# Optimization experiments

Hardware: AMD Instinct MI355X
Metric: run time of the kernel (lower is better)

Reference implementation:

```python
import jax, jax.numpy as jnp
import numpy as np

N_NODES = 50000
N_EDGES = 800000
LEAKY_SLOPE = 0.01
DROPOUT_P = 0.5


def _graph_conv(src, dst, x, W, b):
    """DGL GraphConv with norm='both': D_out^{-1/2} A D_in^{-1/2} X W + b."""
    n = x.shape[0]
    ones = jnp.ones((src.shape[0],), dtype=x.dtype)
    deg_out = jax.ops.segment_sum(ones, src, num_segments=n)  # out-degree of src nodes
    deg_in = jax.ops.segment_sum(ones, dst, num_segments=n)   # in-degree of dst nodes
    norm_src = jax.lax.rsqrt(jnp.maximum(deg_out, 1.0))
    norm_dst = jax.lax.rsqrt(jnp.maximum(deg_in, 1.0))
    h = (x * norm_src[:, None]) @ W          # apply weight before aggregation
    agg = jax.ops.segment_sum(h[src], dst, num_segments=n)  # SpMM aggregate
    return agg * norm_dst[:, None] + b


def _dropout(x, key, p=DROPOUT_P):
    keep = jax.random.bernoulli(key, 1.0 - p, x.shape)
    return jnp.where(keep, x / (1.0 - p), jnp.zeros((), x.dtype))


def setup_inputs() -> dict:
    key = jax.random.key(0)
    ks = jax.random.split(key, 8)
    features = jax.random.normal(ks[0], (N_NODES, 128), dtype=jnp.float32)
    src = jax.random.randint(ks[1], (N_EDGES,), 0, N_NODES, dtype=jnp.int64)
    dst = jax.random.randint(ks[2], (N_EDGES,), 0, N_NODES, dtype=jnp.int64)
    s1 = 1.0 / np.sqrt(128.0)
    s3 = 1.0 / np.sqrt(128.0)
    W1 = jax.random.normal(ks[3], (128, 128), dtype=jnp.float32) * s1
    W2 = jax.random.normal(ks[4], (128, 128), dtype=jnp.float32) * s1
    W3 = jax.random.normal(ks[5], (128, 64), dtype=jnp.float32) * s3
    b1 = jnp.zeros((128,), dtype=jnp.float32)
    b2 = jnp.zeros((128,), dtype=jnp.float32)
    b3 = jnp.zeros((64,), dtype=jnp.float32)
    return {"features": features, "src": src, "dst": dst,
            "W1": W1, "b1": b1, "W2": W2, "b2": b2, "W3": W3, "b3": b3}


def reference(features, src, dst, W1, b1, W2, b2, W3, b3):
    dk = jax.random.split(jax.random.key(42), 3)
    h = jax.nn.leaky_relu(_graph_conv(src, dst, features, W1, b1), LEAKY_SLOPE)
    h = _dropout(h, dk[0])
    h = jax.nn.leaky_relu(_graph_conv(src, dst, h, W2, b2), LEAKY_SLOPE)
    h = _dropout(h, dk[1])
    h = jax.nn.leaky_relu(_graph_conv(src, dst, h, W3, b3), LEAKY_SLOPE)
    h = _dropout(h, dk[2])
    return h
```

## Files before the change

kernel.cpp:

```cpp
#include <hip/hip_runtime.h>
#include <hip/hip_fp16.h>
#include <stdint.h>

using half8 = __attribute__((ext_vector_type(8))) _Float16;
using f32x4 = __attribute__((ext_vector_type(4))) float;

#define SLOT_CAP 64
#define LDW 136
#define NBINS 50176
#define LWORDS 12544
#define NCHUNK 128

#define TFR(r) { x0 += x1; x1 = (x1 << r) | (x1 >> (32 - r)); x1 ^= x0; }

__host__ __device__ inline void threefry2x32(uint32_t k0, uint32_t k1,
                                             uint32_t c0, uint32_t c1,
                                             uint32_t& o0, uint32_t& o1) {
  uint32_t ks2 = k0 ^ k1 ^ 0x1BD11BDAu;
  uint32_t x0 = c0 + k0, x1 = c1 + k1;
  TFR(13) TFR(15) TFR(26) TFR(6)  x0 += k1;  x1 += ks2 + 1u;
  TFR(17) TFR(29) TFR(16) TFR(24) x0 += ks2; x1 += k0 + 2u;
  TFR(13) TFR(15) TFR(26) TFR(6)  x0 += k0;  x1 += k1 + 3u;
  TFR(17) TFR(29) TFR(16) TFR(24) x0 += k1;  x1 += ks2 + 4u;
  TFR(13) TFR(15) TFR(26) TFR(6)  x0 += ks2; x1 += k0 + 5u;
  o0 = x0; o1 = x1;
}

__device__ inline float tf_uniform(uint32_t k0, uint32_t k1, uint32_t i) {
  uint32_t o0, o1;
  threefry2x32(k0, k1, 0u, i, o0, o1);
  uint32_t bits = o0 ^ o1;
  return __uint_as_float((bits >> 9) | 0x3F800000u) - 1.0f;
}

__device__ inline uint16_t f2h(float f) {
  union { _Float16 h; uint16_t u; } c; c.h = (_Float16)f; return c.u;
}
__device__ inline uint32_t pack2h(float a, float b) {
  return (uint32_t)f2h(a) | ((uint32_t)f2h(b) << 16);
}
__device__ inline __half2 u2h2(uint32_t u) {
  union { uint32_t u; __half2 h; } c; c.u = u; return c.h;
}

__device__ inline void hacc(__half2* a, uint4 r) {
  a[0] = __hadd2(a[0], u2h2(r.x));
  a[1] = __hadd2(a[1], u2h2(r.y));
  a[2] = __hadd2(a[2], u2h2(r.z));
  a[3] = __hadd2(a[3], u2h2(r.w));
}

#define GDECL \
  uint4 A0, A1, A2, A3, A4, A5, A6, A7, B0, B1, B2, B3, B4, B5, B6, B7, \
        C0, C1, C2, C3, C4, C5, C6, C7, D0, D1, D2, D3, D4, D5, D6, D7;

#define GPTRS(sl, P) \
  const uint16_t* P##0 = hb + ((size_t)((sl).x & 0xFFFFu) << 7); \
  const uint16_t* P##1 = hb + ((size_t)((sl).x >> 16) << 7);     \
  const uint16_t* P##2 = hb + ((size_t)((sl).y & 0xFFFFu) << 7); \
  const uint16_t* P##3 = hb + ((size_t)((sl).y >> 16) << 7);     \
  const uint16_t* P##4 = hb + ((size_t)((sl).z & 0xFFFFu) << 7); \
  const uint16_t* P##5 = hb + ((size_t)((sl).z >> 16) << 7);     \
  const uint16_t* P##6 = hb + ((size_t)((sl).w & 0xFFFFu) << 7); \
  const uint16_t* P##7 = hb + ((size_t)((sl).w >> 16) << 7);

#define GLOAD(P, X, Y) \
  X##0 = *(const uint4*)P##0; Y##0 = *(const uint4*)(P##0 + 8); \
  X##1 = *(const uint4*)P##1; Y##1 = *(const uint4*)(P##1 + 8); \
  X##2 = *(const uint4*)P##2; Y##2 = *(const uint4*)(P##2 + 8); \
  X##3 = *(const uint4*)P##3; Y##3 = *(const uint4*)(P##3 + 8); \
  X##4 = *(const uint4*)P##4; Y##4 = *(const uint4*)(P##4 + 8); \
  X##5 = *(const uint4*)P##5; Y##5 = *(const uint4*)(P##5 + 8); \
  X##6 = *(const uint4*)P##6; Y##6 = *(const uint4*)(P##6 + 8); \
  X##7 = *(const uint4*)P##7; Y##7 = *(const uint4*)(P##7 + 8);

#define GHACC(X, Y) \
  hacc(ha, X##0); hacc(ha + 4, Y##0); \
  hacc(ha, X##1); hacc(ha + 4, Y##1); \
  hacc(ha, X##2); hacc(ha + 4, Y##2); \
  hacc(ha, X##3); hacc(ha + 4, Y##3); \
  hacc(ha, X##4); hacc(ha + 4, Y##4); \
  hacc(ha, X##5); hacc(ha + 4, Y##5); \
  hacc(ha, X##6); hacc(ha + 4, Y##6); \
  hacc(ha, X##7); hacc(ha + 4, Y##7);

#define ODECL uint4 A0, A1, A2, A3, A4, A5, A6, A7, C0, C1, C2, C3, C4, C5, C6, C7;

#define OPTRS(sl, P) \
  const uint16_t* P##0 = hb + ((size_t)((sl).x & 0xFFFFu) << 6); \
  const uint16_t* P##1 = hb + ((size_t)((sl).x >> 16) << 6);     \
  const uint16_t* P##2 = hb + ((size_t)((sl).y & 0xFFFFu) << 6); \
  const uint16_t* P##3 = hb + ((size_t)((sl).y >> 16) << 6);     \
  const uint16_t* P##4 = hb + ((size_t)((sl).z & 0xFFFFu) << 6); \
  const uint16_t* P##5 = hb + ((size_t)((sl).z >> 16) << 6);     \
  const uint16_t* P##6 = hb + ((size_t)((sl).w & 0xFFFFu) << 6); \
  const uint16_t* P##7 = hb + ((size_t)((sl).w >> 16) << 6);

#define OLOAD(P, X) \
  X##0 = *(const uint4*)P##0; X##1 = *(const uint4*)P##1; \
  X##2 = *(const uint4*)P##2; X##3 = *(const uint4*)P##3; \
  X##4 = *(const uint4*)P##4; X##5 = *(const uint4*)P##5; \
  X##6 = *(const uint4*)P##6; X##7 = *(const uint4*)P##7;

#define OHACC(X) \
  hacc(ha, X##0); hacc(ha, X##1); hacc(ha, X##2); hacc(ha, X##3); \
  hacc(ha, X##4); hacc(ha, X##5); hacc(ha, X##6); hacc(ha, X##7);

__global__ __launch_bounds__(256) void build_hist_kernel(
    const int* __restrict__ src, const int* __restrict__ dst,
    uint16_t* __restrict__ histD, uint16_t* __restrict__ histS,
    uint16_t* __restrict__ rank,
    const float* __restrict__ W1, const float* __restrict__ W2,
    const float* __restrict__ W3, uint16_t* __restrict__ Wt,
    uint16_t* __restrict__ edge_slots,
    int n, int nE, int HR, int EPB) {
  const int bid = (int)blockIdx.x;
  if (bid >= 672) {
    const uint32_t pk = ((uint32_t)n << 16) | (uint32_t)(n & 0xFFFF);
    uint4 f; f.x = pk; f.y = pk; f.z = pk; f.w = pk;
    uint4* es4 = (uint4*)edge_slots;
    const int total = n * (SLOT_CAP / 8);
    for (int i = (bid - 672) * 256 + (int)threadIdx.x; i < total; i += 256 * 256)
      es4[i] = f;
    return;
  }
  if (bid >= 512) {
    int i = (bid - 512) * 256 + (int)threadIdx.x;
    float v;
    if (i < 16384) {
      int nr = i >> 7, k = i & 127;
      v = W1[k * 128 + nr];
    } else if (i < 32768) {
      int j = i - 16384, nr = j >> 7, k = j & 127;
      v = W2[k * 128 + nr];
    } else if (i < 40960) {
      int j = i - 32768, nr = j >> 7, k = j & 127;
      v = W3[k * 64 + nr];
    } else return;
    Wt[i] = f2h(v);
    return;
  }

  __shared__ uint32_t bins[LWORDS];
  const bool isSrc = bid >= 256;
  const int c = bid & 127;
  const int h = (bid >> 7) & 1;
  const int lo = h * HR;
  const int* keys = isSrc ? src : dst;
  uint16_t* hist = isSrc ? histS : histD;

  for (int i = threadIdx.x; i < LWORDS; i += 256) bins[i] = 0u;
  __syncthreads();

  const int e0 = c * EPB, e1 = min(e0 + EPB, nE);
  if (isSrc) {
    for (int e = e0 + (int)threadIdx.x; e < e1; e += 256) {
      int k = keys[e] - lo;
      if ((unsigned)k < (unsigned)HR)
        atomicAdd(&bins[k >> 1], 1u << ((k & 1) * 16));
    }
  } else {
    for (int e = e0 + (int)threadIdx.x; e < e1; e += 256) {
      int k = keys[e] - lo;
      if ((unsigned)k < (unsigned)HR) {
        uint32_t old = atomicAdd(&bins[k >> 1], 1u << ((k & 1) * 16));
        rank[e] = (uint16_t)((old >> ((k & 1) * 16)) & 0xFFFFu);
      }
    }
  }
  __syncthreads();

  uint32_t* out = (uint32_t*)(hist + (size_t)c * NBINS + lo);
  const int wlim = (min(HR, n - lo) + 1) >> 1;
  for (int i = threadIdx.x; i < wlim; i += 256) out[i] = bins[i];
}

__global__ __launch_bounds__(256) void reduce_kernel(
    uint16_t* __restrict__ histD, const uint16_t* __restrict__ histS,
    int* __restrict__ degin, float* __restrict__ nsrc, int n) {
  const int v = blockIdx.x * 256 + (int)threadIdx.x;
  if (v >= n) return;
  uint32_t run = 0;
  #pragma unroll 4
  for (int c = 0; c < NCHUNK; ++c) {
    size_t idx = (size_t)c * NBINS + v;
    uint16_t x = histD[idx];
    histD[idx] = (uint16_t)run;
    run += x;
  }
  degin[v] = (int)run;
  uint32_t s = 0;
  #pragma unroll 4
  for (int c = 0; c < NCHUNK; ++c) s += histS[(size_t)c * NBINS + v];
  nsrc[v] = rsqrtf(fmaxf((float)s, 1.0f));
}

__global__ __launch_bounds__(256) void scatter_gemm1_kernel(
    const int* __restrict__ src, const int* __restrict__ dst,
    const uint16_t* __restrict__ cumD, const uint16_t* __restrict__ rank,
    uint16_t* __restrict__ edge_slots,
    const float* __restrict__ X, const float* __restrict__ nsrc,
    const uint16_t* __restrict__ Wt1, uint16_t* __restrict__ h1,
    int n, int nE, int EPB) {
  const int bid = (int)blockIdx.x;

  if (bid < NCHUNK) {
    const int c = bid;
    const uint16_t* cum = cumD + (size_t)c * NBINS;
    const int e0 = c * EPB, e1 = min(e0 + EPB, nE);
    for (int e = e0 + (int)threadIdx.x; e < e1; e += 256) {
      const int d = dst[e];
      const int pos = (int)cum[d] + (int)rank[e];
      if (pos < SLOT_CAP) edge_slots[((size_t)d << 6) + pos] = (uint16_t)src[e];
    }
    return;
  }

  const int r0 = (bid - NCHUNK) * 64;
  const int tid = (int)threadIdx.x;
  const int wave = tid >> 6, lane = tid & 63;
  const int wm = wave & 1, wn = wave >> 1;
  const int lane15 = lane & 15, quad = lane >> 4;

  const int rowA0 = r0 + wm * 32 + lane15;
  const int rowA1 = rowA0 + 16;
  const bool v0 = rowA0 < n, v1 = rowA1 < n;

  f32x4 acc[2][4] = {};
  #pragma unroll
  for (int kc = 0; kc < 128; kc += 32) {
    const int ko = kc + quad * 8;
    half8 a0 = {}, a1 = {};
    if (v0) {
      float4 x0 = *(const float4*)&X[(size_t)rowA0 * 128 + ko];
      float4 x1 = *(const float4*)&X[(size_t)rowA0 * 128 + ko + 4];
      a0[0] = (_Float16)x0.x; a0[1] = (_Float16)x0.y;
      a0[2] = (_Float16)x0.z; a0[3] = (_Float16)x0.w;
      a0[4] = (_Float16)x1.x; a0[5] = (_Float16)x1.y;
      a0[6] = (_Float16)x1.z; a0[7] = (_Float16)x1.w;
    }
    if (v1) {
      float4 x0 = *(const float4*)&X[(size_t)rowA1 * 128 + ko];
      float4 x1 = *(const float4*)&X[(size_t)rowA1 * 128 + ko + 4];
      a1[0] = (_Float16)x0.x; a1[1] = (_Float16)x0.y;
      a1[2] = (_Float16)x0.z; a1[3] = (_Float16)x0.w;
      a1[4] = (_Float16)x1.x; a1[5] = (_Float16)x1.y;
      a1[6] = (_Float16)x1.z; a1[7] = (_Float16)x1.w;
    }
    #pragma unroll
    for (int nt = 0; nt < 4; ++nt) {
      int nn = wn * 64 + nt * 16 + lane15;
      half8 b = *(const half8*)&Wt1[nn * 128 + ko];
      acc[0][nt] = __builtin_amdgcn_mfma_f32_16x16x32_f16(a0, b, acc[0][nt], 0, 0, 0);
      acc[1][nt] = __builtin_amdgcn_mfma_f32_16x16x32_f16(a1, b, acc[1][nt], 0, 0, 0);
    }
  }

  #pragma unroll
  for (int mt = 0; mt < 2; ++mt) {
    #pragma unroll
    for (int reg = 0; reg < 4; ++reg) {
      int row = r0 + wm * 32 + mt * 16 + quad * 4 + reg;
      float nsr = (row < n) ? nsrc[row] : 0.0f;
      #pragma unroll
      for (int nt = 0; nt < 4; ++nt) {
        int col = wn * 64 + nt * 16 + lane15;
        h1[(size_t)row * 128 + col] = f2h(acc[mt][nt][reg] * nsr);
      }
    }
  }
}

template<int NCOLS>
__global__ __launch_bounds__(256, 3) void fuse_gather_gemm_kernel(
    const uint16_t* __restrict__ h_in, const int* __restrict__ degin,
    const uint16_t* __restrict__ edge_slots, const float* __restrict__ nsrc,
    const float* __restrict__ bias, const uint16_t* __restrict__ Wt,
    uint16_t* __restrict__ h_out, uint32_t k0, uint32_t k1, int n) {
  __shared__ uint16_t Xs[32 * LDW];
  __shared__ float ns_s[32];
  const int r0 = (int)blockIdx.x * 32;
  const int tid = (int)threadIdx.x;

  if (tid < 32) {
    int row = r0 + tid;
    ns_s[tid] = (row < n) ? nsrc[row] : 1.0f;
  }

  const int nl = tid >> 3;
  const int node = r0 + nl;
  const int c16 = (tid & 7) * 16;

  if (node < n) {
    __half2 ha[8];
    #pragma unroll
    for (int j = 0; j < 8; ++j) ha[j] = __half2(__float2half(0.f), __float2half(0.f));

    const int dgi = degin[node];
    const int deg = min(dgi, SLOT_CAP);
    const uint16_t* slots = edge_slots + ((size_t)node << 6);
    const uint16_t* hb = h_in + c16;
    const int nb = (deg + 7) >> 3;

    GDECL
    if (nb > 0) {
      uint4 sA = *(const uint4*)&slots[0];
      GPTRS(sA, p)
      GLOAD(p, A, B)
      int b = 1;
      for (; b + 1 < nb; b += 2) {
        uint4 sB = *(const uint4*)&slots[b * 8];
        uint4 sC = *(const uint4*)&slots[b * 8 + 8];
        GPTRS(sB, q)
        GLOAD(q, C, D)
        GHACC(A, B)
        GPTRS(sC, r)
        GLOAD(r, A, B)
        GHACC(C, D)
      }
      if (b < nb) {
        uint4 sB = *(const uint4*)&slots[b * 8];
        GPTRS(sB, q)
        GLOAD(q, C, D)
        GHACC(A, B)
        GHACC(C, D)
      } else {
        GHACC(A, B)
      }
    }

    float acc[16];
    #pragma unroll
    for (int j = 0; j < 8; ++j) {
      float2 f = __half22float2(ha[j]);
      acc[2 * j] = f.x; acc[2 * j + 1] = f.y;
    }

    const float nd = rsqrtf(fmaxf((float)dgi, 1.0f));
    const float4 b0 = *(const float4*)&bias[c16];
    const float4 b1 = *(const float4*)&bias[c16 + 4];
    const float4 b2 = *(const float4*)&bias[c16 + 8];
    const float4 b3 = *(const float4*)&bias[c16 + 12];
    const float bb[16] = {b0.x, b0.y, b0.z, b0.w, b1.x, b1.y, b1.z, b1.w,
                          b2.x, b2.y, b2.z, b2.w, b3.x, b3.y, b3.z, b3.w};
    const uint32_t i0 = (uint32_t)(node * 128 + c16);

    float o[16];
    #pragma unroll
    for (int j = 0; j < 16; ++j) {
      float v = acc[j] * nd + bb[j];
      v = (v >= 0.f) ? v : 0.01f * v;
      o[j] = (tf_uniform(k0, k1, i0 + (uint32_t)j) < 0.5f) ? v * 2.0f : 0.0f;
    }

    uint4 w0, w1;
    w0.x = pack2h(o[0], o[1]);   w0.y = pack2h(o[2], o[3]);
    w0.z = pack2h(o[4], o[5]);   w0.w = pack2h(o[6], o[7]);
    w1.x = pack2h(o[8], o[9]);   w1.y = pack2h(o[10], o[11]);
    w1.z = pack2h(o[12], o[13]); w1.w = pack2h(o[14], o[15]);
    *(uint4*)&Xs[nl * LDW + c16] = w0;
    *(uint4*)&Xs[nl * LDW + c16 + 8] = w1;
  } else {
    uint4 z = make_uint4(0u, 0u, 0u, 0u);
    *(uint4*)&Xs[nl * LDW + c16] = z;
    *(uint4*)&Xs[nl * LDW + c16 + 8] = z;
  }
  __syncthreads();

  const int wave = tid >> 6, lane = tid & 63;
  const int wm = wave & 1, wn = wave >> 1;
  const int lane15 = lane & 15, quad = lane >> 4;
  constexpr int NT = NCOLS / 32;

  f32x4 acc[NT] = {};
  #pragma unroll
  for (int kc = 0; kc < 128; kc += 32) {
    const int ko = kc + quad * 8;
    half8 a = *(const half8*)&Xs[(wm * 16 + lane15) * LDW + ko];
    #pragma unroll
    for (int nt = 0; nt < NT; ++nt) {
      int nn = wn * (NCOLS / 2) + nt * 16 + lane15;
      half8 b = *(const half8*)&Wt[nn * 128 + ko];
      acc[nt] = __builtin_amdgcn_mfma_f32_16x16x32_f16(a, b, acc[nt], 0, 0, 0);
    }
  }

  #pragma unroll
  for (int nt = 0; nt < NT; ++nt) {
    #pragma unroll
    for (int reg = 0; reg < 4; ++reg) {
      int rl = wm * 16 + quad * 4 + reg;
      int row = r0 + rl;
      int col = wn * (NCOLS / 2) + nt * 16 + lane15;
      h_out[(size_t)row * NCOLS + col] = f2h(acc[nt][reg] * ns_s[rl]);
    }
  }
}

__global__ __launch_bounds__(256, 4) void gather_out_kernel(
    const uint16_t* __restrict__ h3, const int* __restrict__ degin,
    const uint16_t* __restrict__ edge_slots, const float* __restrict__ bias,
    float* __restrict__ out, uint32_t k0, uint32_t k1, int n) {
  const int node = (int)blockIdx.x * 32 + (int)(threadIdx.x >> 3);
  if (node >= n) return;
  const int c8 = (threadIdx.x & 7) * 8;

  const int dgi = degin[node];
  const int deg = min(dgi, SLOT_CAP);
  const uint16_t* slots = edge_slots + ((size_t)node << 6);
  const uint16_t* hb = h3 + c8;
  const int nb = (deg + 7) >> 3;

  __half2 ha[4];
  #pragma unroll
  for (int j = 0; j < 4; ++j) ha[j] = __half2(__float2half(0.f), __float2half(0.f));

  ODECL
  if (nb > 0) {
    uint4 sA = *(const uint4*)&slots[0];
    OPTRS(sA, p)
    OLOAD(p, A)
    int b = 1;
    for (; b + 1 < nb; b += 2) {
      uint4 sB = *(const uint4*)&slots[b * 8];
      uint4 sC = *(const uint4*)&slots[b * 8 + 8];
      OPTRS(sB, q)
      OLOAD(q, C)
      OHACC(A)
      OPTRS(sC, r)
      OLOAD(r, A)
      OHACC(C)
    }
    if (b < nb) {
      uint4 sB = *(const uint4*)&slots[b * 8];
      OPTRS(sB, q)
      OLOAD(q, C)
      OHACC(A)
      OHACC(C)
    } else {
      OHACC(A)
    }
  }

  float acc[8];
  #pragma unroll
  for (int j = 0; j < 4; ++j) {
    float2 f = __half22float2(ha[j]);
    acc[2 * j] = f.x; acc[2 * j + 1] = f.y;
  }

  const float nd = rsqrtf(fmaxf((float)dgi, 1.0f));
  const float4 b0 = *(const float4*)&bias[c8];
  const float4 b1 = *(const float4*)&bias[c8 + 4];
  const float bb[8] = {b0.x, b0.y, b0.z, b0.w, b1.x, b1.y, b1.z, b1.w};
  const uint32_t i0 = (uint32_t)(node * 64 + c8);

  float o[8];
  #pragma unroll
  for (int j = 0; j < 8; ++j) {
    float v = acc[j] * nd + bb[j];
    v = (v >= 0.f) ? v : 0.01f * v;
    o[j] = (tf_uniform(k0, k1, i0 + (uint32_t)j) < 0.5f) ? v * 2.0f : 0.0f;
  }

  float* op = &out[(size_t)node * 64 + c8];
  *(float4*)op = make_float4(o[0], o[1], o[2], o[3]);
  *(float4*)(op + 4) = make_float4(o[4], o[5], o[6], o[7]);
}

extern "C" void kernel_launch(void* const* d_in, const int* in_sizes, int n_in,
                              void* d_out, int out_size, void* d_ws, size_t ws_size,
                              hipStream_t stream) {
  const float* features = (const float*)d_in[0];
  const int*   src      = (const int*)d_in[1];
  const int*   dst      = (const int*)d_in[2];
  const float* W1       = (const float*)d_in[3];
  const float* b1       = (const float*)d_in[4];
  const float* W2       = (const float*)d_in[5];
  const float* b2       = (const float*)d_in[6];
  const float* W3       = (const float*)d_in[7];
  const float* b3       = (const float*)d_in[8];
  float* out = (float*)d_out;

  const int n  = in_sizes[0] / 128;
  const int nE = in_sizes[1];
  const int nA = ((n + 63) / 64) * 64;

  char* p = (char*)d_ws;
  uint16_t* histD      = (uint16_t*)p; p += (size_t)NCHUNK * NBINS * 2;
  uint16_t* histS      = (uint16_t*)p; p += (size_t)NCHUNK * NBINS * 2;
  uint16_t* rank       = (uint16_t*)p; p += (size_t)nE * 2;
  int* degin           = (int*)p;      p += (size_t)n * 4;
  float* nsrc          = (float*)p;    p += (size_t)n * 4;
  uint16_t* edge_slots = (uint16_t*)p; p += (size_t)n * SLOT_CAP * 2;
  uint16_t* Wt         = (uint16_t*)p; p += 40960 * 2;
  uint16_t* h1         = (uint16_t*)p; p += (size_t)nA * 128 * 2;
  uint16_t* h2         = (uint16_t*)p; p += (size_t)nA * 128 * 2;
  uint16_t* h3         = (uint16_t*)p;

  uint32_t dk[3][2];
  for (uint32_t i = 0; i < 3; ++i)
    threefry2x32(0u, 42u, 0u, i, dk[i][0], dk[i][1]);

  const int EPB = (nE + NCHUNK - 1) / NCHUNK;
  int HR = ((n + 3) / 2) & ~1;
  if (HR > 2 * LWORDS) HR = 2 * LWORDS;
  const int gb64 = (n + 63) / 64;
  const int gb32 = (n + 31) / 32;

  build_hist_kernel<<<928, 256, 0, stream>>>(src, dst, histD, histS, rank,
                                             W1, W2, W3, Wt, edge_slots,
                                             n, nE, HR, EPB);
  reduce_kernel<<<(n + 255) / 256, 256, 0, stream>>>(histD, histS, degin, nsrc, n);
  scatter_gemm1_kernel<<<NCHUNK + gb64, 256, 0, stream>>>(
      src, dst, histD, rank, edge_slots, features, nsrc, Wt, h1, n, nE, EPB);
  fuse_gather_gemm_kernel<128><<<gb32, 256, 0, stream>>>(
      h1, degin, edge_slots, nsrc, b1, Wt + 16384, h2, dk[0][0], dk[0][1], n);
  fuse_gather_gemm_kernel<64><<<gb32, 256, 0, stream>>>(
      h2, degin, edge_slots, nsrc, b2, Wt + 32768, h3, dk[1][0], dk[1][1], n);
  gather_out_kernel<<<gb32, 256, 0, stream>>>(
      h3, degin, edge_slots, b3, out, dk[2][0], dk[2][1], n);
}
```

Before: 248.6 us.

## Pack per-chunk degree histograms and ranks into 8-bit counters

Per-chunk histogram bins and per-edge ranks go from 16-bit to 8-bit. The whole node range now fits in one shared-memory array per block, so each chunk needs one histogram block instead of two half-range blocks, and each block reads its edges once instead of twice. The reduce kernel now handles four nodes per thread using 32-bit loads and vector stores. This halves histogram and rank traffic. In exchange it assumes no node gets more than 255 edges in one chunk; prefix sums saturate at 255, which is harmless given the 64-slot cap.

```diff
diff --git a/kernel.cpp b/kernel.cpp
--- a/kernel.cpp
+++ b/kernel.cpp
@@ -8,7 +8,7 @@
 #define SLOT_CAP 64
 #define LDW 136
 #define NBINS 50176
-#define LWORDS 12544
+#define NB32 12544
 #define NCHUNK 128
 
 #define TFR(r) { x0 += x1; x1 = (x1 << r) | (x1 >> (32 - r)); x1 ^= x0; }
@@ -108,24 +108,24 @@
 
 __global__ __launch_bounds__(256) void build_hist_kernel(
     const int* __restrict__ src, const int* __restrict__ dst,
-    uint16_t* __restrict__ histD, uint16_t* __restrict__ histS,
-    uint16_t* __restrict__ rank,
+    uint8_t* __restrict__ histD8, uint8_t* __restrict__ histS8,
+    uint8_t* __restrict__ rank8,
     const float* __restrict__ W1, const float* __restrict__ W2,
     const float* __restrict__ W3, uint16_t* __restrict__ Wt,
     uint16_t* __restrict__ edge_slots,
-    int n, int nE, int HR, int EPB) {
+    int n, int nE, int EPB) {
   const int bid = (int)blockIdx.x;
-  if (bid >= 672) {
+  if (bid >= 416) {
     const uint32_t pk = ((uint32_t)n << 16) | (uint32_t)(n & 0xFFFF);
     uint4 f; f.x = pk; f.y = pk; f.z = pk; f.w = pk;
     uint4* es4 = (uint4*)edge_slots;
     const int total = n * (SLOT_CAP / 8);
-    for (int i = (bid - 672) * 256 + (int)threadIdx.x; i < total; i += 256 * 256)
+    for (int i = (bid - 416) * 256 + (int)threadIdx.x; i < total; i += 256 * 256)
       es4[i] = f;
     return;
   }
-  if (bid >= 512) {
-    int i = (bid - 512) * 256 + (int)threadIdx.x;
+  if (bid >= 256) {
+    int i = (bid - 256) * 256 + (int)threadIdx.x;
     float v;
     if (i < 16384) {
       int nr = i >> 7, k = i & 127;
@@ -141,63 +141,79 @@
     return;
   }
 
-  __shared__ uint32_t bins[LWORDS];
-  const bool isSrc = bid >= 256;
+  __shared__ uint32_t bins[NB32];
+  const bool isSrc = bid >= 128;
   const int c = bid & 127;
-  const int h = (bid >> 7) & 1;
-  const int lo = h * HR;
-  const int* keys = isSrc ? src : dst;
-  uint16_t* hist = isSrc ? histS : histD;
-
-  for (int i = threadIdx.x; i < LWORDS; i += 256) bins[i] = 0u;
+
+  for (int i = threadIdx.x; i < NB32; i += 256) bins[i] = 0u;
   __syncthreads();
 
   const int e0 = c * EPB, e1 = min(e0 + EPB, nE);
   if (isSrc) {
     for (int e = e0 + (int)threadIdx.x; e < e1; e += 256) {
-      int k = keys[e] - lo;
-      if ((unsigned)k < (unsigned)HR)
-        atomicAdd(&bins[k >> 1], 1u << ((k & 1) * 16));
+      const int k = src[e];
+      atomicAdd(&bins[k >> 2], 1u << ((k & 3) * 8));
     }
   } else {
     for (int e = e0 + (int)threadIdx.x; e < e1; e += 256) {
-      int k = keys[e] - lo;
-      if ((unsigned)k < (unsigned)HR) {
-        uint32_t old = atomicAdd(&bins[k >> 1], 1u << ((k & 1) * 16));
-        rank[e] = (uint16_t)((old >> ((k & 1) * 16)) & 0xFFFFu);
-      }
+      const int k = dst[e];
+      const uint32_t old = atomicAdd(&bins[k >> 2], 1u << ((k & 3) * 8));
+      rank8[e] = (uint8_t)((old >> ((k & 3) * 8)) & 0xFFu);
     }
   }
   __syncthreads();
 
-  uint32_t* out = (uint32_t*)(hist + (size_t)c * NBINS + lo);
-  const int wlim = (min(HR, n - lo) + 1) >> 1;
-  for (int i = threadIdx.x; i < wlim; i += 256) out[i] = bins[i];
+  uint32_t* out = (uint32_t*)((isSrc ? histS8 : histD8) + (size_t)c * NBINS);
+  for (int i = threadIdx.x; i < NB32; i += 256) out[i] = bins[i];
 }
 
 __global__ __launch_bounds__(256) void reduce_kernel(
-    uint16_t* __restrict__ histD, const uint16_t* __restrict__ histS,
+    uint8_t* __restrict__ histD8, const uint8_t* __restrict__ histS8,
     int* __restrict__ degin, float* __restrict__ nsrc, int n) {
-  const int v = blockIdx.x * 256 + (int)threadIdx.x;
+  const int v = ((int)blockIdx.x * 256 + (int)threadIdx.x) * 4;
   if (v >= n) return;
-  uint32_t run = 0;
+
+  uint32_t r0 = 0, r1 = 0, r2 = 0, r3 = 0;
   #pragma unroll 4
   for (int c = 0; c < NCHUNK; ++c) {
-    size_t idx = (size_t)c * NBINS + v;
-    uint16_t x = histD[idx];
-    histD[idx] = (uint16_t)run;
-    run += x;
-  }
-  degin[v] = (int)run;
-  uint32_t s = 0;
+    uint32_t* p = (uint32_t*)(histD8 + (size_t)c * NBINS + v);
+    const uint32_t w = *p;
+    *p = min(r0, 255u) | (min(r1, 255u) << 8) |
+         (min(r2, 255u) << 16) | (min(r3, 255u) << 24);
+    r0 += w & 0xFFu; r1 += (w >> 8) & 0xFFu;
+    r2 += (w >> 16) & 0xFFu; r3 += (w >> 24) & 0xFFu;
+  }
+  if (v + 3 < n) {
+    *(int4*)&degin[v] = make_int4((int)r0, (int)r1, (int)r2, (int)r3);
+  } else {
+    const uint32_t rr[4] = {r0, r1, r2, r3};
+    for (int j = 0; v + j < n; ++j) degin[v + j] = (int)rr[j];
+  }
+
+  uint32_t s0 = 0, s1 = 0, s2 = 0, s3 = 0;
   #pragma unroll 4
-  for (int c = 0; c < NCHUNK; ++c) s += histS[(size_t)c * NBINS + v];
-  nsrc[v] = rsqrtf(fmaxf((float)s, 1.0f));
+  for (int c = 0; c < NCHUNK; ++c) {
+    const uint32_t w = *(const uint32_t*)(histS8 + (size_t)c * NBINS + v);
+    s0 += w & 0xFFu; s1 += (w >> 8) & 0xFFu;
+    s2 += (w >> 16) & 0xFFu; s3 += (w >> 24) & 0xFFu;
+  }
+  if (v + 3 < n) {
+    float4 f;
+    f.x = rsqrtf(fmaxf((float)s0, 1.0f));
+    f.y = rsqrtf(fmaxf((float)s1, 1.0f));
+    f.z = rsqrtf(fmaxf((float)s2, 1.0f));
+    f.w = rsqrtf(fmaxf((float)s3, 1.0f));
+    *(float4*)&nsrc[v] = f;
+  } else {
+    const uint32_t ss[4] = {s0, s1, s2, s3};
+    for (int j = 0; v + j < n; ++j)
+      nsrc[v + j] = rsqrtf(fmaxf((float)ss[j], 1.0f));
+  }
 }
 
 __global__ __launch_bounds__(256) void scatter_gemm1_kernel(
     const int* __restrict__ src, const int* __restrict__ dst,
-    const uint16_t* __restrict__ cumD, const uint16_t* __restrict__ rank,
+    const uint8_t* __restrict__ cum8, const uint8_t* __restrict__ rank8,
     uint16_t* __restrict__ edge_slots,
     const float* __restrict__ X, const float* __restrict__ nsrc,
     const uint16_t* __restrict__ Wt1, uint16_t* __restrict__ h1,
@@ -206,11 +222,11 @@
 
   if (bid < NCHUNK) {
     const int c = bid;
-    const uint16_t* cum = cumD + (size_t)c * NBINS;
+    const uint8_t* cum = cum8 + (size_t)c * NBINS;
     const int e0 = c * EPB, e1 = min(e0 + EPB, nE);
     for (int e = e0 + (int)threadIdx.x; e < e1; e += 256) {
       const int d = dst[e];
-      const int pos = (int)cum[d] + (int)rank[e];
+      const int pos = (int)cum[d] + (int)rank8[e];
       if (pos < SLOT_CAP) edge_slots[((size_t)d << 6) + pos] = (uint16_t)src[e];
     }
     return;
@@ -487,9 +503,9 @@
   const int nA = ((n + 63) / 64) * 64;
 
   char* p = (char*)d_ws;
-  uint16_t* histD      = (uint16_t*)p; p += (size_t)NCHUNK * NBINS * 2;
-  uint16_t* histS      = (uint16_t*)p; p += (size_t)NCHUNK * NBINS * 2;
-  uint16_t* rank       = (uint16_t*)p; p += (size_t)nE * 2;
+  uint8_t* histD8      = (uint8_t*)p;  p += (size_t)NCHUNK * NBINS;
+  uint8_t* histS8      = (uint8_t*)p;  p += (size_t)NCHUNK * NBINS;
+  uint8_t* rank8       = (uint8_t*)p;  p += ((size_t)nE + 3) & ~(size_t)3;
   int* degin           = (int*)p;      p += (size_t)n * 4;
   float* nsrc          = (float*)p;    p += (size_t)n * 4;
   uint16_t* edge_slots = (uint16_t*)p; p += (size_t)n * SLOT_CAP * 2;
@@ -503,17 +519,16 @@
     threefry2x32(0u, 42u, 0u, i, dk[i][0], dk[i][1]);
 
   const int EPB = (nE + NCHUNK - 1) / NCHUNK;
-  int HR = ((n + 3) / 2) & ~1;
-  if (HR > 2 * LWORDS) HR = 2 * LWORDS;
   const int gb64 = (n + 63) / 64;
   const int gb32 = (n + 31) / 32;
 
-  build_hist_kernel<<<928, 256, 0, stream>>>(src, dst, histD, histS, rank,
+  build_hist_kernel<<<672, 256, 0, stream>>>(src, dst, histD8, histS8, rank8,
                                              W1, W2, W3, Wt, edge_slots,
-                                             n, nE, HR, EPB);
-  reduce_kernel<<<(n + 255) / 256, 256, 0, stream>>>(histD, histS, degin, nsrc, n);
+                                             n, nE, EPB);
+  reduce_kernel<<<((n + 3) / 4 + 255) / 256, 256, 0, stream>>>(
+      histD8, histS8, degin, nsrc, n);
   scatter_gemm1_kernel<<<NCHUNK + gb64, 256, 0, stream>>>(
-      src, dst, histD, rank, edge_slots, features, nsrc, Wt, h1, n, nE, EPB);
+      src, dst, histD8, rank8, edge_slots, features, nsrc, Wt, h1, n, nE, EPB);
   fuse_gather_gemm_kernel<128><<<gb32, 256, 0, stream>>>(
       h1, degin, edge_slots, nsrc, b1, Wt + 16384, h2, dk[0][0], dk[0][1], n);
   fuse_gather_gemm_kernel<64><<<gb32, 256, 0, stream>>>(
```

Result: no change. 248.7 us (+0.0%).
